# Kernel tuning notes

Measured on AMD Instinct MI355X. Metric: run time of the kernel, lower is better.

The kernel has to match this reference:

```python
import jax, jax.numpy as jnp
import numpy as np
from jax import lax

B, CIN, N = 4, 3, 2048
H, COUT, LEVELS = 128, 3, 3
HEADS = 8

# jnp.convolve(x, f, 'same') with len(f)=8 == correlation with f[::-1], x zero-padded (4,3).
# DWT then takes [::2], which is conv stride 2. IDWT zero-upsamples (lhs_dilation=2) then
# convolves 'same' with f[::-1], i.e. correlation with f, padding (4,4).

def _dwt(x, wlow, whigh):
    # x: (M, L) -> approx, detail each (M, L//2)
    rhs = jnp.stack([wlow[::-1], whigh[::-1]])[:, None, :]  # (2,1,8)
    out = lax.conv_general_dilated(x[:, None, :], rhs, window_strides=(2,),
                                   padding=[(4, 3)],
                                   dimension_numbers=('NCH', 'OIH', 'NCH'))
    return out[:, 0, :], out[:, 1, :]

def _idwt(a, d, wlow, whigh):
    # a, d: (M, L) -> (M, 2L); recon_low + recon_high fused as a 2-in-channel conv
    lhs = jnp.stack([a, d], axis=1)               # (M,2,L)
    rhs = jnp.stack([wlow, whigh])[None, :, :]    # (1,2,8)
    out = lax.conv_general_dilated(lhs, rhs, window_strides=(1,),
                                   padding=[(4, 4)], lhs_dilation=(2,),
                                   dimension_numbers=('NCH', 'OIH', 'NCH'))
    return out[:, 0, :]


def setup_inputs() -> dict:
    key = jax.random.key(0)
    ks = jax.random.split(key, 12)
    db4_low = jnp.array([0.23037781, 0.71484657, 0.63088076, -0.02798376,
                         -0.18703481, 0.03084138, 0.03288301, -0.0105974], jnp.float32)
    db4_high = jnp.array([-0.0105974, -0.03288301, 0.03084138, 0.18703481,
                          -0.02798376, -0.63088076, 0.71484657, -0.23037781], jnp.float32)
    def s(k, shape, fan_in):
        return jax.random.normal(k, shape, jnp.float32) * (1.0 / fan_in) ** 0.5
    return {
        'x': jax.random.normal(ks[0], (B, CIN, N), jnp.float32),
        'wlow': db4_low, 'whigh': db4_high,
        'Win': s(ks[1], (CIN, H), CIN), 'b_in': jnp.zeros((H,), jnp.float32),
        'W1': s(ks[2], (LEVELS, 2, 2 * H), 2), 'b1': jnp.zeros((LEVELS, 2 * H), jnp.float32),
        'W2': s(ks[3], (LEVELS, 2 * H, H), 2 * H), 'b2': jnp.zeros((LEVELS, H), jnp.float32),
        'Wq': s(ks[4], (H, H), H), 'bq': jnp.zeros((H,), jnp.float32),
        'Wk': s(ks[5], (H, H), H), 'bk': jnp.zeros((H,), jnp.float32),
        'Wv': s(ks[6], (H, H), H), 'bv': jnp.zeros((H,), jnp.float32),
        'Wo': s(ks[7], (H, H), H), 'bo': jnp.zeros((H,), jnp.float32),
        'Wout': s(ks[8], (H, COUT), H), 'bout': jnp.zeros((COUT,), jnp.float32),
    }


def reference(x, wlow, whigh, Win, b_in, W1, b1, W2, b2,
              Wq, bq, Wk, bk, Wv, bv, Wo, bo, Wout, bout):
    Bx = x.shape[0]
    # input projection: (B,CIN,N) -> (B,H,N)
    xp = jnp.einsum('bcn,ch->bhn', x, Win) + b_in[None, :, None]
    cur = xp.reshape(Bx * H, N)  # per-(batch,channel) 1D signals, fully batched
    proc = []  # processed coeffs per level; note approx == detail after the shared mean
    for lvl in range(LEVELS):
        a, d = _dwt(cur, wlow, whigh)                 # (M, L)
        c = jnp.stack([a, d], axis=-1)                # (M, L, 2)
        h = jax.nn.gelu(c @ W1[lvl] + b1[lvl])        # (M, L, 2H)
        p = (h @ W2[lvl] + b2[lvl]).mean(axis=-1)     # (M, L): mean over hidden dim
        proc.append(p)
        cur = a
    rec = proc[-1]  # start from deepest processed approx
    for lvl in range(LEVELS - 1, -1, -1):
        rec = _idwt(rec, proc[lvl], wlow, whigh)
    y = rec.reshape(Bx, H, N)
    # cross-level attention: standard MHA with embed_dim=H, 8 heads, no dropout
    seq = y.transpose(0, 2, 1)  # (B,N,H)
    dh = H // HEADS
    q = (seq @ Wq + bq).reshape(Bx, N, HEADS, dh)
    k = (seq @ Wk + bk).reshape(Bx, N, HEADS, dh)
    v = (seq @ Wv + bv).reshape(Bx, N, HEADS, dh)
    att = jnp.einsum('bqhd,bkhd->bhqk', q, k) * (dh ** -0.5)
    att = jax.nn.softmax(att, axis=-1)
    o = jnp.einsum('bhqk,bkhd->bqhd', att, v).reshape(Bx, N, H)
    o = o @ Wo + bo
    out = o @ Wout + bout  # (B,N,COUT)
    return out.transpose(0, 2, 1)  # (B,COUT,N)
```

## Files before the change

### kernel.cpp

```cpp
#include <hip/hip_runtime.h>

#define N_    2048
#define H_    128
#define B_    4
#define CIN_  3
#define COUT_ 3
#define KSPLIT 4
#define LOG2E 1.44269504089f

__device__ __forceinline__ float gelu_tanh(float x) {
    float x2 = x * x;
    float e = __builtin_amdgcn_exp2f(x * fmaf(-0.10294340397f, x2, -2.30220899f));
    return x * __builtin_amdgcn_rcpf(1.0f + e);
}

__global__ void prep_kernel(const float* __restrict__ W2, const float* __restrict__ b2,
                            const float* __restrict__ Wo, const float* __restrict__ bo,
                            const float* __restrict__ Wout, const float* __restrict__ bout,
                            float* __restrict__ w2m, float* __restrict__ b2m,
                            float* __restrict__ wf, float* __restrict__ bf) {
    int gid = blockIdx.x * 256 + threadIdx.x;
    if (gid < 768) {
        const float* r = W2 + (size_t)gid * 128;
        float s = 0.f;
        for (int h = 0; h < 128; ++h) s += r[h];
        w2m[gid] = s * (1.0f / 128.0f);
    } else if (gid < 771) {
        int lvl = gid - 768;
        const float* r = b2 + lvl * 128;
        float s = 0.f;
        for (int h = 0; h < 128; ++h) s += r[h];
        b2m[lvl] = s * (1.0f / 128.0f);
    } else if (gid >= 1024 && gid < 1408) {
        int e = gid - 1024;
        int h = e / 3, c = e - 3 * h;
        float s = 0.f;
        for (int j = 0; j < 128; ++j) s = fmaf(Wo[h * 128 + j], Wout[j * 3 + c], s);
        wf[e] = s;
    } else if (gid >= 1408 && gid < 1411) {
        int c = gid - 1408;
        float s = bout[c];
        for (int j = 0; j < 128; ++j) s = fmaf(bo[j], Wout[j * 3 + c], s);
        bf[c] = s;
    }
}

__global__ __launch_bounds__(256) void xproj_kernel(const float* __restrict__ x,
                                                    const float* __restrict__ Win,
                                                    const float* __restrict__ b_in,
                                                    float* __restrict__ xp) {
    int gid = blockIdx.x * 256 + threadIdx.x;
    int m = gid >> 11;
    int n = gid & 2047;
    int b = m >> 7;
    int h = m & 127;
    const float* xb = x + (size_t)(b * CIN_) * N_ + n;
    float acc = b_in[h];
#pragma unroll
    for (int c = 0; c < CIN_; ++c) acc = fmaf(xb[(size_t)c * N_], Win[c * H_ + h], acc);
    xp[gid] = acc;
}

__global__ __launch_bounds__(256) void dwt_mlp_kernel(
        const float* __restrict__ src, int loSh,
        const float* __restrict__ wlow, const float* __restrict__ whigh,
        const float* __restrict__ W1l, const float* __restrict__ b1l,
        const float* __restrict__ w2ml, const float* __restrict__ b2ml,
        float* __restrict__ a_out, float* __restrict__ p_out) {
    __shared__ float4 wp[256];
    __shared__ float wls[8], whs[8];
    int tid = threadIdx.x;
    wp[tid] = make_float4(W1l[tid], W1l[256 + tid], b1l[tid], w2ml[tid]);
    if (tid < 8) { wls[tid] = wlow[tid]; whs[tid] = whigh[tid]; }
    __syncthreads();

    int gid = blockIdx.x * 256 + tid;
    int Lo  = 1 << loSh;
    int m   = gid >> loSh;
    int i   = gid & (Lo - 1);
    int L   = Lo << 1;
    const float* row = src + (size_t)m * L;
    int j0 = 2 * i - 4;
    float xw[8];
#pragma unroll
    for (int t = 0; t < 8; ++t) {
        int j = j0 + t;
        xw[t] = ((unsigned)j < (unsigned)L) ? row[j] : 0.f;
    }
    float a = 0.f, d = 0.f;
#pragma unroll
    for (int t = 0; t < 8; ++t) {
        a = fmaf(xw[t], wls[7 - t], a);
        d = fmaf(xw[t], whs[7 - t], d);
    }
    float acc = 0.f;
#pragma unroll 8
    for (int kk = 0; kk < 256; ++kk) {
        float4 w = wp[kk];
        float t = fmaf(a, w.x, fmaf(d, w.y, w.z));
        acc = fmaf(gelu_tanh(t), w.w, acc);
    }
    a_out[gid] = a;
    p_out[gid] = acc + b2ml[0];
}

__global__ __launch_bounds__(256) void idwt_kernel(
        const float* __restrict__ aSrc, const float* __restrict__ dSrc,
        int loutSh, const float* __restrict__ wlow, const float* __restrict__ whigh,
        float* __restrict__ out) {
    __shared__ float wls[8], whs[8];
    int tid = threadIdx.x;
    if (tid < 8) { wls[tid] = wlow[tid]; whs[tid] = whigh[tid]; }
    __syncthreads();
    int gid  = blockIdx.x * 256 + tid;
    int Lout = 1 << loutSh;
    int L    = Lout >> 1;
    int m    = gid >> loutSh;
    int ii   = gid & (Lout - 1);
    const float* ar = aSrc + (size_t)m * L;
    const float* dr = dSrc + (size_t)m * L;
    int podd = ii & 1;
    int off0 = (ii >> 1) - 2 + podd;
    float r = 0.f;
#pragma unroll
    for (int s = 0; s < 4; ++s) {
        int idx = off0 + s;
        bool ok = (unsigned)idx < (unsigned)L;
        float av = ok ? ar[idx] : 0.f;
        float dv = ok ? dr[idx] : 0.f;
        r = fmaf(av, wls[2 * s + podd], r);
        r = fmaf(dv, whs[2 * s + podd], r);
    }
    out[gid] = r;
}

__global__ void transpose_kernel(const float* __restrict__ r0, float* __restrict__ seqT) {
    __shared__ float t[32][33];
    int b = blockIdx.z, hT = blockIdx.y, nT = blockIdx.x;
    int tx = threadIdx.x, ty = threadIdx.y;
    int n = nT * 32 + tx;
#pragma unroll
    for (int i = 0; i < 4; ++i) {
        int h = hT * 32 + ty + i * 8;
        t[ty + i * 8][tx] = r0[((size_t)(b * H_ + h)) * N_ + n];
    }
    __syncthreads();
    int h2 = hT * 32 + tx;
#pragma unroll
    for (int i = 0; i < 4; ++i) {
        int n2 = nT * 32 + ty + i * 8;
        seqT[((size_t)(b * N_ + n2)) * H_ + h2] = t[tx][ty + i * 8];
    }
}

__global__ __launch_bounds__(384) void qkv_kernel(
        const float* __restrict__ seqT,
        const float* __restrict__ Wq, const float* __restrict__ bq,
        const float* __restrict__ Wk, const float* __restrict__ bk,
        const float* __restrict__ Wv, const float* __restrict__ bv,
        float* __restrict__ qB, float* __restrict__ kB, float* __restrict__ vB) {
    __shared__ float As[16 * 128];
    int tid = threadIdx.x;
    int rowbase = blockIdx.x * 16;
    for (int idx = tid; idx < 2048; idx += 384)
        As[idx] = seqT[(size_t)rowbase * 128 + idx];
    __syncthreads();

    const float* W; const float* bias; float* dst; int jj;
    if (tid < 128)      { W = Wq; bias = bq; dst = qB; jj = tid; }
    else if (tid < 256) { W = Wk; bias = bk; dst = kB; jj = tid - 128; }
    else                { W = Wv; bias = bv; dst = vB; jj = tid - 256; }

    float acc[16];
#pragma unroll
    for (int r = 0; r < 16; ++r) acc[r] = 0.f;
    for (int h = 0; h < 128; ++h) {
        float w = W[h * 128 + jj];
#pragma unroll
        for (int r = 0; r < 16; ++r) acc[r] = fmaf(As[r * 128 + h], w, acc[r]);
    }
    float bb = bias[jj];
    int head = jj >> 4, t = jj & 15;
    int b  = rowbase >> 11;
    int n0 = rowbase & 2047;
    size_t obase = ((size_t)(b * 8 + head) * N_) * 16 + t;
#pragma unroll
    for (int r = 0; r < 16; ++r)
        dst[obase + (size_t)(n0 + r) * 16] = acc[r] + bb;
}

#define DOT4(acc, qq, aa) do { acc = fmaf(qq.x, aa.x, acc); acc = fmaf(qq.y, aa.y, acc); \
                               acc = fmaf(qq.z, aa.z, acc); acc = fmaf(qq.w, aa.w, acc); } while (0)
#define SCALE4(oo, c)     do { oo.x *= c; oo.y *= c; oo.z *= c; oo.w *= c; } while (0)
#define AXPY4(oo, p, aa)  do { oo.x = fmaf(p, aa.x, oo.x); oo.y = fmaf(p, aa.y, oo.y); \
                               oo.z = fmaf(p, aa.z, oo.z); oo.w = fmaf(p, aa.w, oo.w); } while (0)

__global__ __launch_bounds__(128) void attn_kernel(
        const float* __restrict__ qb, const float* __restrict__ kb,
        const float* __restrict__ vb,
        float* __restrict__ part_o, float* __restrict__ part_ml) {
    __shared__ float4 kt4[256];
    __shared__ float4 vt4[256];
    int tid   = threadIdx.x;
    int blk   = blockIdx.x;
    int split = blk & (KSPLIT - 1);
    int qblk  = (blk >> 2) & 15;
    int bh    = blk >> 6;
    int n     = qblk * 128 + tid;

    const float4* ksrc = (const float4*)(kb + (size_t)bh * N_ * 16);
    const float4* vsrc = (const float4*)(vb + (size_t)bh * N_ * 16);
    const float4* qrow = (const float4*)(qb + ((size_t)bh * N_ + n) * 16);
    float4 q0 = qrow[0], q1 = qrow[1], q2 = qrow[2], q3 = qrow[3];
    const float sc = 0.25f * LOG2E;
    SCALE4(q0, sc); SCALE4(q1, sc); SCALE4(q2, sc); SCALE4(q3, sc);

    float mrun = -3.0e38f, lrun = 0.f;
    float4 o0 = {0,0,0,0}, o1 = o0, o2 = o0, o3 = o0;

    int k0base = split * (N_ / KSPLIT);
    for (int kb0 = k0base; kb0 < k0base + N_ / KSPLIT; kb0 += 64) {
        __syncthreads();
        int src0 = kb0 * 4;
        kt4[tid]       = ksrc[src0 + tid];
        kt4[tid + 128] = ksrc[src0 + tid + 128];
        vt4[tid]       = vsrc[src0 + tid];
        vt4[tid + 128] = vsrc[src0 + tid + 128];
        __syncthreads();

        for (int c0 = 0; c0 < 64; c0 += 32) {
            float sv[32];
            float cmax = -3.0e38f;
#pragma unroll
            for (int c = 0; c < 32; ++c) {
                int kr = (c0 + c) * 4;
                float4 a0 = kt4[kr], a1 = kt4[kr+1], a2 = kt4[kr+2], a3 = kt4[kr+3];
                float sA = 0.f, sB = 0.f;
                DOT4(sA, q0, a0); DOT4(sB, q1, a1);
                DOT4(sA, q2, a2); DOT4(sB, q3, a3);
                sv[c] = sA + sB;
                cmax = fmaxf(cmax, sv[c]);
            }
            float mn   = fmaxf(mrun, cmax);
            float corr = __builtin_amdgcn_exp2f(mrun - mn);
            lrun *= corr;
            SCALE4(o0, corr); SCALE4(o1, corr); SCALE4(o2, corr); SCALE4(o3, corr);
#pragma unroll
            for (int c = 0; c < 32; ++c) {
                float p = __builtin_amdgcn_exp2f(sv[c] - mn);
                lrun += p;
                int vr = (c0 + c) * 4;
                float4 b0 = vt4[vr], b1 = vt4[vr+1], b2 = vt4[vr+2], b3 = vt4[vr+3];
                AXPY4(o0, p, b0); AXPY4(o1, p, b1); AXPY4(o2, p, b2); AXPY4(o3, p, b3);
            }
            mrun = mn;
        }
    }
    int qg = bh * N_ + n;
    float4* po = (float4*)(part_o + ((size_t)split * (32 * N_) + qg) * 16);
    po[0] = o0; po[1] = o1; po[2] = o2; po[3] = o3;
    float2* pm = (float2*)(part_ml + ((size_t)split * (32 * N_) + qg) * 2);
    pm[0] = make_float2(mrun, lrun);
}

__global__ __launch_bounds__(256) void attn_combine_kernel(
        const float* __restrict__ part_o, const float* __restrict__ part_ml,
        float* __restrict__ ot) {
    int qg = blockIdx.x * 256 + threadIdx.x;
    float m[KSPLIT], l[KSPLIT];
    float M = -3.0e38f;
#pragma unroll
    for (int s = 0; s < KSPLIT; ++s) {
        float2 ml = ((const float2*)part_ml)[(size_t)s * (32 * N_) + qg];
        m[s] = ml.x; l[s] = ml.y;
        M = fmaxf(M, m[s]);
    }
    float w[KSPLIT], lt = 0.f;
#pragma unroll
    for (int s = 0; s < KSPLIT; ++s) {
        w[s] = __builtin_amdgcn_exp2f(m[s] - M);
        lt = fmaf(l[s], w[s], lt);
    }
    float inv = __builtin_amdgcn_rcpf(lt);
    float o[16];
#pragma unroll
    for (int j = 0; j < 16; ++j) o[j] = 0.f;
#pragma unroll
    for (int s = 0; s < KSPLIT; ++s) {
        const float4* po = (const float4*)(part_o + ((size_t)s * (32 * N_) + qg) * 16);
#pragma unroll
        for (int r = 0; r < 4; ++r) {
            float4 v = po[r];
            o[4*r+0] = fmaf(v.x, w[s], o[4*r+0]);
            o[4*r+1] = fmaf(v.y, w[s], o[4*r+1]);
            o[4*r+2] = fmaf(v.z, w[s], o[4*r+2]);
            o[4*r+3] = fmaf(v.w, w[s], o[4*r+3]);
        }
    }
    int bh = qg >> 11, n = qg & 2047;
    int b = bh >> 3, head = bh & 7;
    size_t base = ((size_t)(b * H_ + head * 16)) * N_ + n;
#pragma unroll
    for (int j = 0; j < 16; ++j) ot[base + (size_t)j * N_] = o[j] * inv;
}

__global__ __launch_bounds__(256) void final_kernel(
        const float* __restrict__ ot, const float* __restrict__ wf,
        const float* __restrict__ bf, float* __restrict__ out) {
    __shared__ float wfs[384];
    __shared__ float bfs[3];
    int tid = threadIdx.x;
    for (int i = tid; i < 384; i += 256) wfs[i] = wf[i];
    if (tid < 3) bfs[tid] = bf[tid];
    __syncthreads();
    int b = blockIdx.x >> 3;
    int n = (blockIdx.x & 7) * 256 + tid;
    const float* col = ot + (size_t)b * H_ * N_ + n;
    float a0 = 0.f, a1 = 0.f, a2 = 0.f;
#pragma unroll 4
    for (int h = 0; h < 128; ++h) {
        float v = col[(size_t)h * N_];
        a0 = fmaf(v, wfs[h * 3 + 0], a0);
        a1 = fmaf(v, wfs[h * 3 + 1], a1);
        a2 = fmaf(v, wfs[h * 3 + 2], a2);
    }
    size_t ob = ((size_t)b * 3) * N_ + n;
    out[ob]          = a0 + bfs[0];
    out[ob + N_]     = a1 + bfs[1];
    out[ob + 2 * N_] = a2 + bfs[2];
}

extern "C" void kernel_launch(void* const* d_in, const int* in_sizes, int n_in,
                              void* d_out, int out_size, void* d_ws, size_t ws_size,
                              hipStream_t stream) {
    const float* x    = (const float*)d_in[0];
    const float* wlow = (const float*)d_in[1];
    const float* whigh= (const float*)d_in[2];
    const float* Win  = (const float*)d_in[3];
    const float* b_in = (const float*)d_in[4];
    const float* W1   = (const float*)d_in[5];
    const float* b1   = (const float*)d_in[6];
    const float* W2   = (const float*)d_in[7];
    const float* b2   = (const float*)d_in[8];
    const float* Wq   = (const float*)d_in[9];
    const float* bq   = (const float*)d_in[10];
    const float* Wk   = (const float*)d_in[11];
    const float* bk   = (const float*)d_in[12];
    const float* Wv   = (const float*)d_in[13];
    const float* bv   = (const float*)d_in[14];
    const float* Wo   = (const float*)d_in[15];
    const float* bo   = (const float*)d_in[16];
    const float* Wout = (const float*)d_in[17];
    const float* bout = (const float*)d_in[18];
    float* out = (float*)d_out;

    float* ws = (float*)d_ws;
    size_t off = 0;
    auto alloc = [&](size_t nf) { float* p = ws + off; off += nf; return p; };
    float* xp   = alloc(512 * 2048);
    float* a1   = alloc(512 * 1024);
    float* p0   = alloc(512 * 1024);
    float* a2   = alloc(512 * 512);
    float* p1   = alloc(512 * 512);
    float* a3   = alloc(512 * 256);
    float* p2   = alloc(512 * 256);
    float* r2   = alloc(512 * 512);
    float* r1   = alloc(512 * 1024);
    float* r0   = alloc(512 * 2048);
    float* seqT = alloc(4 * 2048 * 128);
    float* qB   = alloc(4 * 8 * 2048 * 16);
    float* kB   = alloc(4 * 8 * 2048 * 16);
    float* vB   = alloc(4 * 8 * 2048 * 16);
    float* otB  = alloc(4 * 128 * 2048);
    float* w2m  = alloc(768);
    float* b2m  = alloc(16);
    float* wf   = alloc(384);
    float* bf   = alloc(16);
    float* part_o  = ws;
    float* part_ml = ws + (size_t)KSPLIT * 65536 * 16;
    (void)ws_size; (void)in_sizes; (void)n_in; (void)out_size;

    prep_kernel<<<8, 256, 0, stream>>>(W2, b2, Wo, bo, Wout, bout, w2m, b2m, wf, bf);
    xproj_kernel<<<4096, 256, 0, stream>>>(x, Win, b_in, xp);

    dwt_mlp_kernel<<<2048, 256, 0, stream>>>(xp, 10, wlow, whigh,
                                             W1 + 0,    b1 + 0,   w2m + 0,   b2m + 0, a1, p0);
    dwt_mlp_kernel<<<1024, 256, 0, stream>>>(a1, 9,  wlow, whigh,
                                             W1 + 512,  b1 + 256, w2m + 256, b2m + 1, a2, p1);
    dwt_mlp_kernel<<<512, 256, 0, stream>>>(a2, 8,  wlow, whigh,
                                             W1 + 1024, b1 + 512, w2m + 512, b2m + 2, a3, p2);

    idwt_kernel<<<1024, 256, 0, stream>>>(p2, p2, 9,  wlow, whigh, r2);
    idwt_kernel<<<2048, 256, 0, stream>>>(r2, p1, 10, wlow, whigh, r1);
    idwt_kernel<<<4096, 256, 0, stream>>>(r1, p0, 11, wlow, whigh, r0);

    dim3 tg(64, 4, 4), tb(32, 8);
    transpose_kernel<<<tg, tb, 0, stream>>>(r0, seqT);
    qkv_kernel<<<512, 384, 0, stream>>>(seqT, Wq, bq, Wk, bk, Wv, bv, qB, kB, vB);
    attn_kernel<<<2048, 128, 0, stream>>>(qB, kB, vB, part_o, part_ml);
    attn_combine_kernel<<<256, 256, 0, stream>>>(part_o, part_ml, otB);
    final_kernel<<<32, 256, 0, stream>>>(otB, wf, bf, out);
}
```

Measured before the change: 391.3 us.

## Fuse projections, transpose and combine kernels; register-block attention with lazy rescale

```diff
diff --git a/kernel.cpp b/kernel.cpp
--- a/kernel.cpp
+++ b/kernel.cpp
@@ -5,7 +5,6 @@
 #define B_    4
 #define CIN_  3
 #define COUT_ 3
-#define KSPLIT 4
 #define LOG2E 1.44269504089f
 
 __device__ __forceinline__ float gelu_tanh(float x) {
@@ -45,24 +44,11 @@
     }
 }
 
-__global__ __launch_bounds__(256) void xproj_kernel(const float* __restrict__ x,
-                                                    const float* __restrict__ Win,
-                                                    const float* __restrict__ b_in,
-                                                    float* __restrict__ xp) {
-    int gid = blockIdx.x * 256 + threadIdx.x;
-    int m = gid >> 11;
-    int n = gid & 2047;
-    int b = m >> 7;
-    int h = m & 127;
-    const float* xb = x + (size_t)(b * CIN_) * N_ + n;
-    float acc = b_in[h];
-#pragma unroll
-    for (int c = 0; c < CIN_; ++c) acc = fmaf(xb[(size_t)c * N_], Win[c * H_ + h], acc);
-    xp[gid] = acc;
-}
-
+template<bool FUSEX>
 __global__ __launch_bounds__(256) void dwt_mlp_kernel(
         const float* __restrict__ src, int loSh,
+        const float* __restrict__ x, const float* __restrict__ Win,
+        const float* __restrict__ b_in,
         const float* __restrict__ wlow, const float* __restrict__ whigh,
         const float* __restrict__ W1l, const float* __restrict__ b1l,
         const float* __restrict__ w2ml, const float* __restrict__ b2ml,
@@ -79,13 +65,31 @@
     int m   = gid >> loSh;
     int i   = gid & (Lo - 1);
     int L   = Lo << 1;
-    const float* row = src + (size_t)m * L;
-    int j0 = 2 * i - 4;
+    int j0  = 2 * i - 4;
     float xw[8];
-#pragma unroll
-    for (int t = 0; t < 8; ++t) {
-        int j = j0 + t;
-        xw[t] = ((unsigned)j < (unsigned)L) ? row[j] : 0.f;
+    if (FUSEX) {
+        int b = m >> 7, h = m & 127;
+        float w0 = Win[h], w1 = Win[128 + h], w2 = Win[256 + h];
+        float bi = b_in[h];
+        const float* xr = x + (size_t)b * (CIN_ * N_);
+#pragma unroll
+        for (int t = 0; t < 8; ++t) {
+            int j = j0 + t;
+            bool ok = (unsigned)j < (unsigned)L;
+            int jc = ok ? j : 0;
+            float v = bi;
+            v = fmaf(xr[jc], w0, v);
+            v = fmaf(xr[N_ + jc], w1, v);
+            v = fmaf(xr[2 * N_ + jc], w2, v);
+            xw[t] = ok ? v : 0.f;
+        }
+    } else {
+        const float* row = src + (size_t)m * L;
+#pragma unroll
+        for (int t = 0; t < 8; ++t) {
+            int j = j0 + t;
+            xw[t] = ((unsigned)j < (unsigned)L) ? row[j] : 0.f;
+        }
     }
     float a = 0.f, d = 0.f;
 #pragma unroll
@@ -134,36 +138,22 @@
     out[gid] = r;
 }
 
-__global__ void transpose_kernel(const float* __restrict__ r0, float* __restrict__ seqT) {
-    __shared__ float t[32][33];
-    int b = blockIdx.z, hT = blockIdx.y, nT = blockIdx.x;
-    int tx = threadIdx.x, ty = threadIdx.y;
-    int n = nT * 32 + tx;
-#pragma unroll
-    for (int i = 0; i < 4; ++i) {
-        int h = hT * 32 + ty + i * 8;
-        t[ty + i * 8][tx] = r0[((size_t)(b * H_ + h)) * N_ + n];
-    }
-    __syncthreads();
-    int h2 = hT * 32 + tx;
-#pragma unroll
-    for (int i = 0; i < 4; ++i) {
-        int n2 = nT * 32 + ty + i * 8;
-        seqT[((size_t)(b * N_ + n2)) * H_ + h2] = t[tx][ty + i * 8];
-    }
-}
-
 __global__ __launch_bounds__(384) void qkv_kernel(
-        const float* __restrict__ seqT,
+        const float* __restrict__ r0,
         const float* __restrict__ Wq, const float* __restrict__ bq,
         const float* __restrict__ Wk, const float* __restrict__ bk,
         const float* __restrict__ Wv, const float* __restrict__ bv,
         float* __restrict__ qB, float* __restrict__ kB, float* __restrict__ vB) {
-    __shared__ float As[16 * 128];
+    __shared__ float As[16 * 130];
     int tid = threadIdx.x;
     int rowbase = blockIdx.x * 16;
-    for (int idx = tid; idx < 2048; idx += 384)
-        As[idx] = seqT[(size_t)rowbase * 128 + idx];
+    int b  = rowbase >> 11;
+    int n0 = rowbase & 2047;
+    for (int idx = tid; idx < 2048; idx += 384) {
+        int h = idx >> 4;
+        int r = idx & 15;
+        As[r * 130 + h] = r0[((size_t)(b * H_ + h)) * N_ + n0 + r];
+    }
     __syncthreads();
 
     const float* W; const float* bias; float* dst; int jj;
@@ -177,12 +167,10 @@
     for (int h = 0; h < 128; ++h) {
         float w = W[h * 128 + jj];
 #pragma unroll
-        for (int r = 0; r < 16; ++r) acc[r] = fmaf(As[r * 128 + h], w, acc[r]);
+        for (int r = 0; r < 16; ++r) acc[r] = fmaf(As[r * 130 + h], w, acc[r]);
     }
     float bb = bias[jj];
     int head = jj >> 4, t = jj & 15;
-    int b  = rowbase >> 11;
-    int n0 = rowbase & 2047;
     size_t obase = ((size_t)(b * 8 + head) * N_) * 16 + t;
 #pragma unroll
     for (int r = 0; r < 16; ++r)
@@ -195,89 +183,114 @@
 #define AXPY4(oo, p, aa)  do { oo.x = fmaf(p, aa.x, oo.x); oo.y = fmaf(p, aa.y, oo.y); \
                                oo.z = fmaf(p, aa.z, oo.z); oo.w = fmaf(p, aa.w, oo.w); } while (0)
 
-__global__ __launch_bounds__(128) void attn_kernel(
+template<int KS>
+__global__ __launch_bounds__(128, 4) void attn_kernel(
         const float* __restrict__ qb, const float* __restrict__ kb,
         const float* __restrict__ vb,
         float* __restrict__ part_o, float* __restrict__ part_ml) {
-    __shared__ float4 kt4[256];
-    __shared__ float4 vt4[256];
+    __shared__ float4 kt4[512];
+    __shared__ float4 vt4[512];
     int tid   = threadIdx.x;
     int blk   = blockIdx.x;
-    int split = blk & (KSPLIT - 1);
-    int qblk  = (blk >> 2) & 15;
-    int bh    = blk >> 6;
-    int n     = qblk * 128 + tid;
-
-    const float4* ksrc = (const float4*)(kb + (size_t)bh * N_ * 16);
-    const float4* vsrc = (const float4*)(vb + (size_t)bh * N_ * 16);
-    const float4* qrow = (const float4*)(qb + ((size_t)bh * N_ + n) * 16);
-    float4 q0 = qrow[0], q1 = qrow[1], q2 = qrow[2], q3 = qrow[3];
+    int split = blk % KS;
+    int qblk  = (blk / KS) & 7;
+    int bh    = blk / (8 * KS);
+    int nA    = qblk * 256 + tid;
+    int nB    = nA + 128;
+
+    const float4* ksrc = (const float4*)(kb + (size_t)bh * (N_ * 16));
+    const float4* vsrc = (const float4*)(vb + (size_t)bh * (N_ * 16));
+    const float4* qra  = (const float4*)(qb + ((size_t)bh * N_ + nA) * 16);
+    const float4* qrb  = (const float4*)(qb + ((size_t)bh * N_ + nB) * 16);
     const float sc = 0.25f * LOG2E;
-    SCALE4(q0, sc); SCALE4(q1, sc); SCALE4(q2, sc); SCALE4(q3, sc);
-
-    float mrun = -3.0e38f, lrun = 0.f;
-    float4 o0 = {0,0,0,0}, o1 = o0, o2 = o0, o3 = o0;
-
-    int k0base = split * (N_ / KSPLIT);
-    for (int kb0 = k0base; kb0 < k0base + N_ / KSPLIT; kb0 += 64) {
+    float4 qa0 = qra[0], qa1 = qra[1], qa2 = qra[2], qa3 = qra[3];
+    float4 qb0 = qrb[0], qb1 = qrb[1], qb2 = qrb[2], qb3 = qrb[3];
+    SCALE4(qa0, sc); SCALE4(qa1, sc); SCALE4(qa2, sc); SCALE4(qa3, sc);
+    SCALE4(qb0, sc); SCALE4(qb1, sc); SCALE4(qb2, sc); SCALE4(qb3, sc);
+
+    float mA = -3.0e38f, lA = 0.f, mB = -3.0e38f, lB = 0.f;
+    float4 oA0 = {0,0,0,0}, oA1 = oA0, oA2 = oA0, oA3 = oA0;
+    float4 oB0 = oA0, oB1 = oA0, oB2 = oA0, oB3 = oA0;
+
+    int k0 = split * (N_ / KS);
+    for (int t0 = k0; t0 < k0 + N_ / KS; t0 += 128) {
         __syncthreads();
-        int src0 = kb0 * 4;
-        kt4[tid]       = ksrc[src0 + tid];
-        kt4[tid + 128] = ksrc[src0 + tid + 128];
-        vt4[tid]       = vsrc[src0 + tid];
-        vt4[tid + 128] = vsrc[src0 + tid + 128];
+        const float4* ks = ksrc + t0 * 4;
+        const float4* vs = vsrc + t0 * 4;
+        kt4[tid] = ks[tid]; kt4[tid+128] = ks[tid+128]; kt4[tid+256] = ks[tid+256]; kt4[tid+384] = ks[tid+384];
+        vt4[tid] = vs[tid]; vt4[tid+128] = vs[tid+128]; vt4[tid+256] = vs[tid+256]; vt4[tid+384] = vs[tid+384];
         __syncthreads();
 
-        for (int c0 = 0; c0 < 64; c0 += 32) {
-            float sv[32];
-            float cmax = -3.0e38f;
-#pragma unroll
-            for (int c = 0; c < 32; ++c) {
+        for (int c0 = 0; c0 < 128; c0 += 8) {
+            float svA[8], svB[8];
+            float cmA = -3.0e38f, cmB = -3.0e38f;
+#pragma unroll
+            for (int c = 0; c < 8; ++c) {
                 int kr = (c0 + c) * 4;
-                float4 a0 = kt4[kr], a1 = kt4[kr+1], a2 = kt4[kr+2], a3 = kt4[kr+3];
-                float sA = 0.f, sB = 0.f;
-                DOT4(sA, q0, a0); DOT4(sB, q1, a1);
-                DOT4(sA, q2, a2); DOT4(sB, q3, a3);
-                sv[c] = sA + sB;
-                cmax = fmaxf(cmax, sv[c]);
+                float4 k0v = kt4[kr], k1v = kt4[kr+1], k2v = kt4[kr+2], k3v = kt4[kr+3];
+                float s0 = 0.f, s1 = 0.f, u0 = 0.f, u1 = 0.f;
+                DOT4(s0, qa0, k0v); DOT4(s1, qa1, k1v); DOT4(s0, qa2, k2v); DOT4(s1, qa3, k3v);
+                DOT4(u0, qb0, k0v); DOT4(u1, qb1, k1v); DOT4(u0, qb2, k2v); DOT4(u1, qb3, k3v);
+                svA[c] = s0 + s1; svB[c] = u0 + u1;
+                cmA = fmaxf(cmA, svA[c]); cmB = fmaxf(cmB, svB[c]);
             }
-            float mn   = fmaxf(mrun, cmax);
-            float corr = __builtin_amdgcn_exp2f(mrun - mn);
-            lrun *= corr;
-            SCALE4(o0, corr); SCALE4(o1, corr); SCALE4(o2, corr); SCALE4(o3, corr);
-#pragma unroll
-            for (int c = 0; c < 32; ++c) {
-                float p = __builtin_amdgcn_exp2f(sv[c] - mn);
-                lrun += p;
+            if (__any((cmA > mA + 8.f) || (cmB > mB + 8.f))) {
+                float mnA = fmaxf(mA, cmA), mnB = fmaxf(mB, cmB);
+                float cA = __builtin_amdgcn_exp2f(mA - mnA);
+                float cB = __builtin_amdgcn_exp2f(mB - mnB);
+                lA *= cA; lB *= cB;
+                SCALE4(oA0, cA); SCALE4(oA1, cA); SCALE4(oA2, cA); SCALE4(oA3, cA);
+                SCALE4(oB0, cB); SCALE4(oB1, cB); SCALE4(oB2, cB); SCALE4(oB3, cB);
+                mA = mnA; mB = mnB;
+            }
+#pragma unroll
+            for (int c = 0; c < 8; ++c) {
+                float pA = __builtin_amdgcn_exp2f(svA[c] - mA);
+                float pB = __builtin_amdgcn_exp2f(svB[c] - mB);
+                lA += pA; lB += pB;
                 int vr = (c0 + c) * 4;
-                float4 b0 = vt4[vr], b1 = vt4[vr+1], b2 = vt4[vr+2], b3 = vt4[vr+3];
-                AXPY4(o0, p, b0); AXPY4(o1, p, b1); AXPY4(o2, p, b2); AXPY4(o3, p, b3);
+                float4 v0 = vt4[vr], v1 = vt4[vr+1], v2 = vt4[vr+2], v3 = vt4[vr+3];
+                AXPY4(oA0, pA, v0); AXPY4(oA1, pA, v1); AXPY4(oA2, pA, v2); AXPY4(oA3, pA, v3);
+                AXPY4(oB0, pB, v0); AXPY4(oB1, pB, v1); AXPY4(oB2, pB, v2); AXPY4(oB3, pB, v3);
             }
-            mrun = mn;
         }
     }
-    int qg = bh * N_ + n;
-    float4* po = (float4*)(part_o + ((size_t)split * (32 * N_) + qg) * 16);
-    po[0] = o0; po[1] = o1; po[2] = o2; po[3] = o3;
-    float2* pm = (float2*)(part_ml + ((size_t)split * (32 * N_) + qg) * 2);
-    pm[0] = make_float2(mrun, lrun);
-}
-
-__global__ __launch_bounds__(256) void attn_combine_kernel(
+    int qgA = bh * N_ + nA, qgB = bh * N_ + nB;
+    float4* poA = (float4*)part_o + ((size_t)split * 65536 + qgA) * 4;
+    poA[0] = oA0; poA[1] = oA1; poA[2] = oA2; poA[3] = oA3;
+    float4* poB = (float4*)part_o + ((size_t)split * 65536 + qgB) * 4;
+    poB[0] = oB0; poB[1] = oB1; poB[2] = oB2; poB[3] = oB3;
+    ((float2*)part_ml)[(size_t)split * 65536 + qgA] = make_float2(mA, lA);
+    ((float2*)part_ml)[(size_t)split * 65536 + qgB] = make_float2(mB, lB);
+}
+
+template<int KS>
+__global__ __launch_bounds__(512) void combine_final_kernel(
         const float* __restrict__ part_o, const float* __restrict__ part_ml,
-        float* __restrict__ ot) {
-    int qg = blockIdx.x * 256 + threadIdx.x;
-    float m[KSPLIT], l[KSPLIT];
+        const float* __restrict__ wf, const float* __restrict__ bf,
+        float* __restrict__ out) {
+    __shared__ float ysh[64 * 129];
+    __shared__ float wfs[384];
+    __shared__ float bfs[3];
+    int tid = threadIdx.x;
+    if (tid < 384) wfs[tid] = wf[tid];
+    if (tid >= 384 && tid < 387) bfs[tid - 384] = bf[tid - 384];
+    int b = blockIdx.x >> 5, nb = blockIdx.x & 31;
+    int head = tid >> 6, nl = tid & 63;
+    int n = nb * 64 + nl;
+    int qg = (b * 8 + head) * N_ + n;
+
+    float m[KS], l[KS];
     float M = -3.0e38f;
 #pragma unroll
-    for (int s = 0; s < KSPLIT; ++s) {
-        float2 ml = ((const float2*)part_ml)[(size_t)s * (32 * N_) + qg];
+    for (int s = 0; s < KS; ++s) {
+        float2 ml = ((const float2*)part_ml)[(size_t)s * 65536 + qg];
         m[s] = ml.x; l[s] = ml.y;
         M = fmaxf(M, m[s]);
     }
-    float w[KSPLIT], lt = 0.f;
-#pragma unroll
-    for (int s = 0; s < KSPLIT; ++s) {
+    float w[KS], lt = 0.f;
+#pragma unroll
+    for (int s = 0; s < KS; ++s) {
         w[s] = __builtin_amdgcn_exp2f(m[s] - M);
         lt = fmaf(l[s], w[s], lt);
     }
@@ -286,8 +299,8 @@
 #pragma unroll
     for (int j = 0; j < 16; ++j) o[j] = 0.f;
 #pragma unroll
-    for (int s = 0; s < KSPLIT; ++s) {
-        const float4* po = (const float4*)(part_o + ((size_t)s * (32 * N_) + qg) * 16);
+    for (int s = 0; s < KS; ++s) {
+        const float4* po = (const float4*)part_o + ((size_t)s * 65536 + qg) * 4;
 #pragma unroll
         for (int r = 0; r < 4; ++r) {
             float4 v = po[r];
@@ -297,37 +310,18 @@
             o[4*r+3] = fmaf(v.w, w[s], o[4*r+3]);
         }
     }
-    int bh = qg >> 11, n = qg & 2047;
-    int b = bh >> 3, head = bh & 7;
-    size_t base = ((size_t)(b * H_ + head * 16)) * N_ + n;
-#pragma unroll
-    for (int j = 0; j < 16; ++j) ot[base + (size_t)j * N_] = o[j] * inv;
-}
-
-__global__ __launch_bounds__(256) void final_kernel(
-        const float* __restrict__ ot, const float* __restrict__ wf,
-        const float* __restrict__ bf, float* __restrict__ out) {
-    __shared__ float wfs[384];
-    __shared__ float bfs[3];
-    int tid = threadIdx.x;
-    for (int i = tid; i < 384; i += 256) wfs[i] = wf[i];
-    if (tid < 3) bfs[tid] = bf[tid];
+    int col = head * 16;
+#pragma unroll
+    for (int j = 0; j < 16; ++j) ysh[nl * 129 + col + j] = o[j] * inv;
     __syncthreads();
-    int b = blockIdx.x >> 3;
-    int n = (blockIdx.x & 7) * 256 + tid;
-    const float* col = ot + (size_t)b * H_ * N_ + n;
-    float a0 = 0.f, a1 = 0.f, a2 = 0.f;
+    if (tid < 192) {
+        int c = tid >> 6, nl2 = tid & 63;
+        float acc = bfs[c];
+        const float* yr = ysh + nl2 * 129;
 #pragma unroll 4
-    for (int h = 0; h < 128; ++h) {
-        float v = col[(size_t)h * N_];
-        a0 = fmaf(v, wfs[h * 3 + 0], a0);
-        a1 = fmaf(v, wfs[h * 3 + 1], a1);
-        a2 = fmaf(v, wfs[h * 3 + 2], a2);
-    }
-    size_t ob = ((size_t)b * 3) * N_ + n;
-    out[ob]          = a0 + bfs[0];
-    out[ob + N_]     = a1 + bfs[1];
-    out[ob + 2 * N_] = a2 + bfs[2];
+        for (int h = 0; h < 128; ++h) acc = fmaf(yr[h], wfs[h * 3 + c], acc);
+        out[((size_t)b * 3 + c) * N_ + nb * 64 + nl2] = acc;
+    }
 }
 
 extern "C" void kernel_launch(void* const* d_in, const int* in_sizes, int n_in,
@@ -353,51 +347,54 @@
     const float* Wout = (const float*)d_in[17];
     const float* bout = (const float*)d_in[18];
     float* out = (float*)d_out;
+    (void)in_sizes; (void)n_in; (void)out_size;
 
     float* ws = (float*)d_ws;
-    size_t off = 0;
-    auto alloc = [&](size_t nf) { float* p = ws + off; off += nf; return p; };
-    float* xp   = alloc(512 * 2048);
-    float* a1   = alloc(512 * 1024);
-    float* p0   = alloc(512 * 1024);
-    float* a2   = alloc(512 * 512);
-    float* p1   = alloc(512 * 512);
-    float* a3   = alloc(512 * 256);
-    float* p2   = alloc(512 * 256);
-    float* r2   = alloc(512 * 512);
-    float* r1   = alloc(512 * 1024);
-    float* r0   = alloc(512 * 2048);
-    float* seqT = alloc(4 * 2048 * 128);
-    float* qB   = alloc(4 * 8 * 2048 * 16);
-    float* kB   = alloc(4 * 8 * 2048 * 16);
-    float* vB   = alloc(4 * 8 * 2048 * 16);
-    float* otB  = alloc(4 * 128 * 2048);
-    float* w2m  = alloc(768);
-    float* b2m  = alloc(16);
-    float* wf   = alloc(384);
-    float* bf   = alloc(16);
-    float* part_o  = ws;
-    float* part_ml = ws + (size_t)KSPLIT * 65536 * 16;
-    (void)ws_size; (void)in_sizes; (void)n_in; (void)out_size;
+    float* qBuf  = ws;
+    float* kBuf  = ws + 1048576;
+    float* vBuf  = ws + 2097152;
+    float* base2 = ws + 3145728;
+    float* a1 = base2;
+    float* p0 = base2 + 524288;
+    float* a2 = base2 + 1048576;
+    float* p1 = base2 + 1310720;
+    float* a3 = base2 + 1572864;
+    float* p2 = base2 + 1703936;
+    float* r2 = base2 + 1835008;
+    float* r1 = base2 + 2097152;
+    float* r0 = base2 + 2621440;
+
+    const size_t need8 = (3145728ull + 8ull * 1048576 + 8ull * 131072 + 2048ull) * 4;
+    int KS = (ws_size >= need8) ? 8 : 4;
+
+    float* part_o  = base2;
+    float* part_ml = base2 + (size_t)KS * 1048576;
+    float* smalls  = part_ml + (size_t)KS * 131072;
+    float* w2m = smalls;
+    float* b2m = smalls + 768;
+    float* wf  = smalls + 771;
+    float* bf  = smalls + 1155;
 
     prep_kernel<<<8, 256, 0, stream>>>(W2, b2, Wo, bo, Wout, bout, w2m, b2m, wf, bf);
-    xproj_kernel<<<4096, 256, 0, stream>>>(x, Win, b_in, xp);
-
-    dwt_mlp_kernel<<<2048, 256, 0, stream>>>(xp, 10, wlow, whigh,
-                                             W1 + 0,    b1 + 0,   w2m + 0,   b2m + 0, a1, p0);
-    dwt_mlp_kernel<<<1024, 256, 0, stream>>>(a1, 9,  wlow, whigh,
-                                             W1 + 512,  b1 + 256, w2m + 256, b2m + 1, a2, p1);
-    dwt_mlp_kernel<<<512, 256, 0, stream>>>(a2, 8,  wlow, whigh,
-                                             W1 + 1024, b1 + 512, w2m + 512, b2m + 2, a3, p2);
+
+    dwt_mlp_kernel<true><<<2048, 256, 0, stream>>>(nullptr, 10, x, Win, b_in, wlow, whigh,
+                                                   W1 + 0,    b1 + 0,   w2m + 0,   b2m + 0, a1, p0);
+    dwt_mlp_kernel<false><<<1024, 256, 0, stream>>>(a1, 9, nullptr, nullptr, nullptr, wlow, whigh,
+                                                    W1 + 512,  b1 + 256, w2m + 256, b2m + 1, a2, p1);
+    dwt_mlp_kernel<false><<<512, 256, 0, stream>>>(a2, 8, nullptr, nullptr, nullptr, wlow, whigh,
+                                                   W1 + 1024, b1 + 512, w2m + 512, b2m + 2, a3, p2);
 
     idwt_kernel<<<1024, 256, 0, stream>>>(p2, p2, 9,  wlow, whigh, r2);
     idwt_kernel<<<2048, 256, 0, stream>>>(r2, p1, 10, wlow, whigh, r1);
     idwt_kernel<<<4096, 256, 0, stream>>>(r1, p0, 11, wlow, whigh, r0);
 
-    dim3 tg(64, 4, 4), tb(32, 8);
-    transpose_kernel<<<tg, tb, 0, stream>>>(r0, seqT);
-    qkv_kernel<<<512, 384, 0, stream>>>(seqT, Wq, bq, Wk, bk, Wv, bv, qB, kB, vB);
-    attn_kernel<<<2048, 128, 0, stream>>>(qB, kB, vB, part_o, part_ml);
-    attn_combine_kernel<<<256, 256, 0, stream>>>(part_o, part_ml, otB);
-    final_kernel<<<32, 256, 0, stream>>>(otB, wf, bf, out);
-}
+    qkv_kernel<<<512, 384, 0, stream>>>(r0, Wq, bq, Wk, bk, Wv, bv, qBuf, kBuf, vBuf);
+
+    if (KS == 8) {
+        attn_kernel<8><<<32 * 8 * 8, 128, 0, stream>>>(qBuf, kBuf, vBuf, part_o, part_ml);
+        combine_final_kernel<8><<<128, 512, 0, stream>>>(part_o, part_ml, wf, bf, out);
+    } else {
+        attn_kernel<4><<<32 * 8 * 4, 128, 0, stream>>>(qBuf, kBuf, vBuf, part_o, part_ml);
+        combine_final_kernel<4><<<128, 512, 0, stream>>>(part_o, part_ml, wf, bf, out);
+    }
+}
```

New measurement: 372.2 us. 1.05x faster.
